# Kernel tuning notes

Hardware: AMD Instinct MI355X
Metric: run time of the kernel (lower is better)

## Reference

```python
import jax, jax.numpy as jnp
import numpy as np

B, NA, T, NV, D = 24, 50, 10, 196, 512


def setup_inputs() -> dict:
    key = jax.random.key(0)
    k1, k2 = jax.random.split(key)
    return {
        "audio_feats": jax.random.normal(k1, (B, NA, D), dtype=jnp.float32),
        "visual_feats": jax.random.normal(k2, (B, T, NV, D), dtype=jnp.float32),
        "temperature": jnp.float32(2.5),
        "scale_factor": jnp.float32(2.5),
        "threshold": jnp.float32(-2.5),
    }


def _l2norm(x):
    # F.normalize(dim=-1): x / max(||x||, 1e-12)
    n = jnp.sqrt(jnp.sum(x * x, axis=-1, keepdims=True))
    return x / jnp.maximum(n, 1e-12)


def reference(audio_feats, visual_feats, temperature, scale_factor, threshold):
    b = audio_feats.shape[0]
    a = _l2norm(audio_feats)          # (B,Na,D)
    v = _l2norm(visual_feats)         # (B,T,Nv,D)
    # all-pairs token similarities: (B,B,Na,T,Nv)
    sims = jnp.einsum('xad,ytvd->xyatv', a, v) / temperature

    # aggregate_temporal_similarities
    th = jax.nn.sigmoid(threshold)
    max_vis = jnp.max(sims, axis=-1)            # (B,B,Na,T)
    raw_diff = max_vis - th
    sel = jax.nn.relu(raw_diff) * scale_factor  # selection strength
    weighted_sum = jnp.sum(max_vis * sel, axis=-1)   # over T
    weights_sum = jnp.sum(sel, axis=-1)
    token_sims = weighted_sum / jnp.maximum(weights_sum, 1e-6)
    clip_sims = jnp.mean(token_sims, axis=-1)   # (B,B)
    fraction_selected = jnp.mean((raw_diff > 0).astype(jnp.float32))

    # InfoNCE
    idx = jnp.arange(b)
    losses_a2v = -jax.nn.log_softmax(clip_sims, axis=1)[idx, idx]
    losses_v2a = -jax.nn.log_softmax(clip_sims.T, axis=1)[idx, idx]
    contrastive_loss = jnp.mean(losses_a2v + losses_v2a) / 2

    # regularization
    neg = jnp.clip(sims, -20.0, 0.0)
    l_nonneg = jnp.mean(neg * neg)
    temp_low = jnp.maximum(-jnp.log(temperature), 0.0) ** 2   # log(1)=0
    temp_high = jnp.maximum(jnp.log(temperature) - jnp.log(4.0), 0.0) ** 2
    l_cal = temp_low + temp_high
    l_threshold = jnp.maximum(th - 0.9, 0.0) ** 2 + jnp.maximum(0.1 - th, 0.0) ** 2
    l_scale = jnp.maximum(scale_factor - 20.0, 0.0) ** 2 + jnp.maximum(1.0 - scale_factor, 0.0) ** 2
    reg_loss = 0.15 * l_nonneg + 2.0 * l_cal + 0.1 * l_threshold + 0.1 * l_scale

    # selection reward on positive pairs (diagonal)
    pos_diffs = raw_diff[idx, idx]                       # (B,Na,T)
    sel_ratio = (jnp.tanh(20.0 * pos_diffs) + 1.0) / 2.0
    selection_reward = -0.1 * jnp.log1p(jnp.mean(sel_ratio))

    total_loss = selection_reward + contrastive_loss + reg_loss
    return (total_loss, contrastive_loss, reg_loss, fraction_selected, selection_reward)
```

## Files before the change

### kernel.cpp

```cpp
#include <hip/hip_runtime.h>
#include <math.h>

#define B_   24
#define NA_  50
#define T_   10
#define NV_  196
#define D_   512
#define M_   1200
#define MPAD 1280
#define NVP  224
#define YT_  240
#define VROWS (YT_ * NVP)
#define CHB  22528

typedef __bf16 bf16x8 __attribute__((ext_vector_type(8)));
typedef float  f32x4  __attribute__((ext_vector_type(4)));
typedef unsigned short ushort8 __attribute__((ext_vector_type(8)));

__device__ __forceinline__ unsigned short f2bf(float f) {
    unsigned u = __float_as_uint(f);
    u += 0x7FFF + ((u >> 16) & 1);
    return (unsigned short)(u >> 16);
}

__device__ __forceinline__ void gload16(const void* g, void* l) {
    __builtin_amdgcn_global_load_lds(
        (const __attribute__((address_space(1))) unsigned int*)g,
        (__attribute__((address_space(3))) unsigned int*)l, 16, 0, 0);
}

__global__ void normconv_kernel(const float* __restrict__ vf, const float* __restrict__ af,
                                const float* __restrict__ tempPtr,
                                unsigned short* __restrict__ Vbf, unsigned short* __restrict__ Abf,
                                float* __restrict__ accs) {
    if (blockIdx.x == 0 && threadIdx.x < 3) accs[threadIdx.x] = 0.0f;
    int w = threadIdx.x >> 6, lane = threadIdx.x & 63;
    int row = blockIdx.x * 4 + w;
    const float* p = nullptr;
    unsigned short* dstp;
    float tscale = 1.0f;
    if (row < VROWS) {
        int yt = row / NVP, vv = row - yt * NVP;
        dstp = Vbf + (size_t)row * D_;
        if (vv < NV_) p = vf + ((size_t)yt * NV_ + vv) * D_;
    } else {
        int ar = row - VROWS;
        if (ar >= MPAD) return;
        dstp = Abf + (size_t)ar * D_;
        if (ar < M_) { p = af + (size_t)ar * D_; tscale = tempPtr[0]; }
    }
    ushort8* dst = (ushort8*)(dstp + lane * 8);
    if (p) {
        float4 u = *(const float4*)(p + lane * 8);
        float4 v = *(const float4*)(p + lane * 8 + 4);
        float s = u.x*u.x + u.y*u.y + u.z*u.z + u.w*u.w
                + v.x*v.x + v.y*v.y + v.z*v.z + v.w*v.w;
        #pragma unroll
        for (int off = 32; off; off >>= 1) s += __shfl_xor(s, off, 64);
        float sc = 1.0f / (fmaxf(sqrtf(s), 1e-12f) * tscale);
        ushort8 o;
        o[0]=f2bf(u.x*sc); o[1]=f2bf(u.y*sc); o[2]=f2bf(u.z*sc); o[3]=f2bf(u.w*sc);
        o[4]=f2bf(v.x*sc); o[5]=f2bf(v.y*sc); o[6]=f2bf(v.z*sc); o[7]=f2bf(v.w*sc);
        *dst = o;
    } else {
        ushort8 z = (ushort8)0;
        *dst = z;
    }
}

__global__ __launch_bounds__(256) void simred_kernel(
    const unsigned short* __restrict__ Abf, const unsigned short* __restrict__ Vbf,
    float* __restrict__ maxvis, float* __restrict__ accNonneg)
{
    __shared__ __align__(16) unsigned char lds[CHB];
    __shared__ float maxred[2][128];
    __shared__ float redbuf[4];

    const int tid  = threadIdx.x;
    const int lane = tid & 63;
    const int w    = tid >> 6;
    const int q    = lane >> 4;
    const int m16  = lane & 15;
    const int wr   = w & 1;
    const int wc   = w >> 1;

    const int flat = blockIdx.x + gridDim.x * blockIdx.y;
    const int xcd  = flat & 7;
    const int slot = flat >> 3;
    const int grp  = slot / 10;
    const int rt   = slot - grp * 10;
    const int yt   = xcd * 30 + grp;
    const int rowA0 = rt * 128;
    const size_t vRow0 = (size_t)yt * NVP;

    const unsigned short* gp[6];
    int lpOff[6];
    int nun = 0;
    #pragma unroll
    for (int i = 0; i < 6; ++i) {
        int u = w + 4 * i;
        if (u < 22) {
            if (u < 8) gp[nun] = Abf + (size_t)(rowA0 + u * 16 + m16) * D_ + q * 8;
            else       gp[nun] = Vbf + (vRow0 + (size_t)((u - 8) * 16 + m16)) * D_ + q * 8;
            lpOff[nun] = u * 1024;
            ++nun;
        }
    }

    int aOff[4], bOff[7];
    #pragma unroll
    for (int i = 0; i < 4; ++i) aOff[i] = (wr * 4 + i) * 1024 + q * 256 + m16 * 16;
    #pragma unroll
    for (int j = 0; j < 7; ++j) bOff[j] = 8192 + (wc * 7 + j) * 1024 + q * 256 + m16 * 16;

    f32x4 acc[4][7];
    #pragma unroll
    for (int i = 0; i < 4; ++i)
        #pragma unroll
        for (int j = 0; j < 7; ++j) acc[i][j] = (f32x4)0.0f;

    for (int c = 0; c < 16; ++c) {
        __syncthreads();
        #pragma unroll
        for (int i = 0; i < 6; ++i)
            if (i < nun) gload16(gp[i] + c * 32, lds + lpOff[i]);
        __syncthreads();
        bf16x8 afr[4], bfr[7];
        #pragma unroll
        for (int i = 0; i < 4; ++i) afr[i] = *(const bf16x8*)(lds + aOff[i]);
        #pragma unroll
        for (int j = 0; j < 7; ++j) bfr[j] = *(const bf16x8*)(lds + bOff[j]);
        #pragma unroll
        for (int i = 0; i < 4; ++i)
            #pragma unroll
            for (int j = 0; j < 7; ++j)
                acc[i][j] = __builtin_amdgcn_mfma_f32_16x16x32_bf16(afr[i], bfr[j], acc[i][j], 0, 0, 0);
    }

    float cs = 0.0f;
    #pragma unroll
    for (int i = 0; i < 4; ++i)
        #pragma unroll
        for (int j = 0; j < 7; ++j)
            #pragma unroll
            for (int r = 0; r < 4; ++r) {
                float v = acc[i][j][r];
                float cv = fminf(fmaxf(v, -20.0f), 0.0f);
                cs += cv * cv;
            }
    #pragma unroll
    for (int off = 32; off; off >>= 1) cs += __shfl_xor(cs, off, 64);
    if (lane == 0) redbuf[w] = cs;

    bool colv[7];
    #pragma unroll
    for (int j = 0; j < 7; ++j) colv[j] = (wc * 112 + j * 16 + m16) < NV_;
    #pragma unroll
    for (int i = 0; i < 4; ++i) {
        float mx[4] = {-3e38f, -3e38f, -3e38f, -3e38f};
        #pragma unroll
        for (int j = 0; j < 7; ++j)
            #pragma unroll
            for (int r = 0; r < 4; ++r)
                mx[r] = fmaxf(mx[r], colv[j] ? acc[i][j][r] : -3e38f);
        #pragma unroll
        for (int r = 0; r < 4; ++r) {
            float mm = mx[r];
            #pragma unroll
            for (int off = 1; off <= 8; off <<= 1) mm = fmaxf(mm, __shfl_xor(mm, off, 64));
            if (m16 == 0) maxred[wc][wr * 64 + i * 16 + q * 4 + r] = mm;
        }
    }
    __syncthreads();
    if (tid == 0) atomicAdd(accNonneg, redbuf[0] + redbuf[1] + redbuf[2] + redbuf[3]);
    if (tid < 128) {
        float mm = fmaxf(maxred[0][tid], maxred[1][tid]);
        int R = rowA0 + tid;
        if (R < M_) {
            int x = R / NA_, a = R - x * NA_;
            int y = yt / T_, t = yt - y * T_;
            maxvis[(((size_t)x * B_ + y) * NA_ + a) * T_ + t] = mm;
        }
    }
}

__global__ void aggregate_kernel(const float* __restrict__ maxvis,
                                 const float* __restrict__ thrPtr,
                                 const float* __restrict__ scalePtr,
                                 float* __restrict__ clipSims,
                                 float* __restrict__ accFrac,
                                 float* __restrict__ accSel)
{
    int xy = blockIdx.x;
    int x = xy / B_, y = xy % B_;
    int a = threadIdx.x;
    float th    = 1.0f / (1.0f + expf(-thrPtr[0]));
    float scale = scalePtr[0];
    float token = 0.0f, cnt = 0.0f, selsum = 0.0f;
    if (a < NA_) {
        const float* p = maxvis + (((size_t)x * B_ + y) * NA_ + a) * T_;
        float ws = 0.0f, ss = 0.0f;
        #pragma unroll
        for (int t = 0; t < T_; ++t) {
            float mv  = p[t];
            float rd  = mv - th;
            float sel = fmaxf(rd, 0.0f) * scale;
            ws += mv * sel;
            ss += sel;
            if (rd > 0.0f) cnt += 1.0f;
            if (x == y) selsum += 0.5f * (tanhf(20.0f * rd) + 1.0f);
        }
        token = ws / fmaxf(ss, 1e-6f);
    }
    #pragma unroll
    for (int off = 32; off; off >>= 1) {
        token  += __shfl_xor(token,  off, 64);
        cnt    += __shfl_xor(cnt,    off, 64);
        selsum += __shfl_xor(selsum, off, 64);
    }
    if (threadIdx.x == 0) {
        clipSims[x * B_ + y] = token / (float)NA_;
        atomicAdd(accFrac, cnt);
        if (x == y) atomicAdd(accSel, selsum);
    }
}

__global__ void finalize_kernel(const float* __restrict__ clipSims,
                                const float* __restrict__ accs,
                                const float* __restrict__ tempPtr,
                                const float* __restrict__ scalePtr,
                                const float* __restrict__ thrPtr,
                                float* __restrict__ out)
{
    __shared__ float cs[B_ * B_];
    int tid = threadIdx.x;
    for (int i = tid; i < B_ * B_; i += 64) cs[i] = clipSims[i];
    __syncthreads();
    float lsum = 0.0f;
    if (tid < B_) {
        int i = tid;
        float m = -1e30f;
        for (int j = 0; j < B_; ++j) m = fmaxf(m, cs[i * B_ + j]);
        float e = 0.0f;
        for (int j = 0; j < B_; ++j) e += expf(cs[i * B_ + j] - m);
        float la = m + logf(e) - cs[i * B_ + i];
        float m2 = -1e30f;
        for (int j = 0; j < B_; ++j) m2 = fmaxf(m2, cs[j * B_ + i]);
        float e2 = 0.0f;
        for (int j = 0; j < B_; ++j) e2 += expf(cs[j * B_ + i] - m2);
        float lv = m2 + logf(e2) - cs[i * B_ + i];
        lsum = la + lv;
    }
    #pragma unroll
    for (int off = 32; off; off >>= 1) lsum += __shfl_xor(lsum, off, 64);
    if (tid == 0) {
        float contrastive = lsum / (float)B_ * 0.5f;
        float temp = tempPtr[0], scl = scalePtr[0];
        float th = 1.0f / (1.0f + expf(-thrPtr[0]));
        float l_nonneg = accs[0] / 56448000.0f;
        float logt = logf(temp);
        float tl  = fmaxf(-logt, 0.0f);
        float thi = fmaxf(logt - logf(4.0f), 0.0f);
        float l_cal = tl * tl + thi * thi;
        float t1 = fmaxf(th - 0.9f, 0.0f), t2 = fmaxf(0.1f - th, 0.0f);
        float l_thr = t1 * t1 + t2 * t2;
        float s1 = fmaxf(scl - 20.0f, 0.0f), s2 = fmaxf(1.0f - scl, 0.0f);
        float l_scale = s1 * s1 + s2 * s2;
        float reg = 0.15f * l_nonneg + 2.0f * l_cal + 0.1f * l_thr + 0.1f * l_scale;
        float frac   = accs[1] / 288000.0f;
        float selrew = -0.1f * log1pf(accs[2] / 12000.0f);
        out[0] = selrew + contrastive + reg;
        out[1] = contrastive;
        out[2] = reg;
        out[3] = frac;
        out[4] = selrew;
    }
}

extern "C" void kernel_launch(void* const* d_in, const int* in_sizes, int n_in,
                              void* d_out, int out_size, void* d_ws, size_t ws_size,
                              hipStream_t stream) {
    const float* audio  = (const float*)d_in[0];
    const float* visual = (const float*)d_in[1];
    const float* temp   = (const float*)d_in[2];
    const float* scale  = (const float*)d_in[3];
    const float* thr    = (const float*)d_in[4];
    float* out = (float*)d_out;

    unsigned char* wsb = (unsigned char*)d_ws;
    unsigned short* Abf = (unsigned short*)wsb;
    unsigned short* Vbf = (unsigned short*)(wsb + 1310720);
    float* maxvis   = (float*)(wsb + 1310720 + 55050240);
    float* clipSims = (float*)(wsb + 1310720 + 55050240 + 1152000);
    float* accs     = clipSims + 576;

    normconv_kernel<<<(VROWS + MPAD) / 4, 256, 0, stream>>>(visual, audio, temp, Vbf, Abf, accs);

    dim3 grid(MPAD / 128, YT_);
    simred_kernel<<<grid, 256, 0, stream>>>(Abf, Vbf, maxvis, accs);

    aggregate_kernel<<<B_ * B_, 64, 0, stream>>>(maxvis, thr, scale, clipSims, accs + 1, accs + 2);
    finalize_kernel<<<1, 64, 0, stream>>>(clipSims, accs, temp, scale, thr, out);
}
```

Measured before the change: 307.6 us.

## Halve simred row tile and prefetch next K-chunk through registers

```diff
diff --git a/kernel.cpp b/kernel.cpp
--- a/kernel.cpp
+++ b/kernel.cpp
@@ -11,7 +11,7 @@
 #define NVP  224
 #define YT_  240
 #define VROWS (YT_ * NVP)
-#define CHB  22528
+#define CHB  18432
 
 typedef __bf16 bf16x8 __attribute__((ext_vector_type(8)));
 typedef float  f32x4  __attribute__((ext_vector_type(4)));
@@ -21,12 +21,6 @@
     unsigned u = __float_as_uint(f);
     u += 0x7FFF + ((u >> 16) & 1);
     return (unsigned short)(u >> 16);
-}
-
-__device__ __forceinline__ void gload16(const void* g, void* l) {
-    __builtin_amdgcn_global_load_lds(
-        (const __attribute__((address_space(1))) unsigned int*)g,
-        (__attribute__((address_space(3))) unsigned int*)l, 16, 0, 0);
 }
 
 __global__ void normconv_kernel(const float* __restrict__ vf, const float* __restrict__ af,
@@ -73,7 +67,7 @@
     float* __restrict__ maxvis, float* __restrict__ accNonneg)
 {
     __shared__ __align__(16) unsigned char lds[CHB];
-    __shared__ float maxred[2][128];
+    __shared__ float maxred[2][64];
     __shared__ float redbuf[4];
 
     const int tid  = threadIdx.x;
@@ -81,57 +75,66 @@
     const int w    = tid >> 6;
     const int q    = lane >> 4;
     const int m16  = lane & 15;
-    const int wr   = w & 1;
-    const int wc   = w >> 1;
-
-    const int flat = blockIdx.x + gridDim.x * blockIdx.y;
+    const int wrow = w >> 1;
+    const int wcol = w & 1;
+
+    const int flat = blockIdx.x;
     const int xcd  = flat & 7;
     const int slot = flat >> 3;
-    const int grp  = slot / 10;
-    const int rt   = slot - grp * 10;
+    const int grp  = slot / 20;
+    const int rt   = slot - grp * 20;
     const int yt   = xcd * 30 + grp;
-    const int rowA0 = rt * 128;
+    const int rowA0 = rt * 64;
     const size_t vRow0 = (size_t)yt * NVP;
 
-    const unsigned short* gp[6];
-    int lpOff[6];
-    int nun = 0;
-    #pragma unroll
-    for (int i = 0; i < 6; ++i) {
+    const unsigned short* gp[5];
+    int lpOff[5];
+    const int nun = (w < 2) ? 5 : 4;
+    #pragma unroll
+    for (int i = 0; i < 5; ++i) {
         int u = w + 4 * i;
-        if (u < 22) {
-            if (u < 8) gp[nun] = Abf + (size_t)(rowA0 + u * 16 + m16) * D_ + q * 8;
-            else       gp[nun] = Vbf + (vRow0 + (size_t)((u - 8) * 16 + m16)) * D_ + q * 8;
-            lpOff[nun] = u * 1024;
-            ++nun;
-        }
-    }
-
-    int aOff[4], bOff[7];
-    #pragma unroll
-    for (int i = 0; i < 4; ++i) aOff[i] = (wr * 4 + i) * 1024 + q * 256 + m16 * 16;
-    #pragma unroll
-    for (int j = 0; j < 7; ++j) bOff[j] = 8192 + (wc * 7 + j) * 1024 + q * 256 + m16 * 16;
-
-    f32x4 acc[4][7];
-    #pragma unroll
-    for (int i = 0; i < 4; ++i)
+        if (u < 18) {
+            if (u < 4) gp[i] = Abf + (size_t)(rowA0 + u * 16 + m16) * D_ + q * 8;
+            else       gp[i] = Vbf + (vRow0 + (size_t)((u - 4) * 16 + m16)) * D_ + q * 8;
+            lpOff[i] = u * 1024 + lane * 16;
+        }
+    }
+
+    int aOff[2], bOff[7];
+    #pragma unroll
+    for (int i = 0; i < 2; ++i) aOff[i] = (wrow * 2 + i) * 1024 + q * 256 + m16 * 16;
+    #pragma unroll
+    for (int j = 0; j < 7; ++j) bOff[j] = 4096 + (wcol * 7 + j) * 1024 + q * 256 + m16 * 16;
+
+    f32x4 acc[2][7];
+    #pragma unroll
+    for (int i = 0; i < 2; ++i)
         #pragma unroll
         for (int j = 0; j < 7; ++j) acc[i][j] = (f32x4)0.0f;
+
+    uint4 stg[5];
+    #pragma unroll
+    for (int i = 0; i < 5; ++i)
+        if (i < nun) stg[i] = *(const uint4*)(gp[i]);
 
     for (int c = 0; c < 16; ++c) {
         __syncthreads();
         #pragma unroll
-        for (int i = 0; i < 6; ++i)
-            if (i < nun) gload16(gp[i] + c * 32, lds + lpOff[i]);
+        for (int i = 0; i < 5; ++i)
+            if (i < nun) *(uint4*)(lds + lpOff[i]) = stg[i];
         __syncthreads();
-        bf16x8 afr[4], bfr[7];
-        #pragma unroll
-        for (int i = 0; i < 4; ++i) afr[i] = *(const bf16x8*)(lds + aOff[i]);
+        if (c < 15) {
+            #pragma unroll
+            for (int i = 0; i < 5; ++i)
+                if (i < nun) stg[i] = *(const uint4*)(gp[i] + (c + 1) * 32);
+        }
+        bf16x8 afr[2], bfr[7];
+        #pragma unroll
+        for (int i = 0; i < 2; ++i) afr[i] = *(const bf16x8*)(lds + aOff[i]);
         #pragma unroll
         for (int j = 0; j < 7; ++j) bfr[j] = *(const bf16x8*)(lds + bOff[j]);
         #pragma unroll
-        for (int i = 0; i < 4; ++i)
+        for (int i = 0; i < 2; ++i)
             #pragma unroll
             for (int j = 0; j < 7; ++j)
                 acc[i][j] = __builtin_amdgcn_mfma_f32_16x16x32_bf16(afr[i], bfr[j], acc[i][j], 0, 0, 0);
@@ -139,7 +142,7 @@
 
     float cs = 0.0f;
     #pragma unroll
-    for (int i = 0; i < 4; ++i)
+    for (int i = 0; i < 2; ++i)
         #pragma unroll
         for (int j = 0; j < 7; ++j)
             #pragma unroll
@@ -154,9 +157,9 @@
 
     bool colv[7];
     #pragma unroll
-    for (int j = 0; j < 7; ++j) colv[j] = (wc * 112 + j * 16 + m16) < NV_;
-    #pragma unroll
-    for (int i = 0; i < 4; ++i) {
+    for (int j = 0; j < 7; ++j) colv[j] = (wcol * 112 + j * 16 + m16) < NV_;
+    #pragma unroll
+    for (int i = 0; i < 2; ++i) {
         float mx[4] = {-3e38f, -3e38f, -3e38f, -3e38f};
         #pragma unroll
         for (int j = 0; j < 7; ++j)
@@ -168,12 +171,12 @@
             float mm = mx[r];
             #pragma unroll
             for (int off = 1; off <= 8; off <<= 1) mm = fmaxf(mm, __shfl_xor(mm, off, 64));
-            if (m16 == 0) maxred[wc][wr * 64 + i * 16 + q * 4 + r] = mm;
+            if (m16 == 0) maxred[wcol][wrow * 32 + i * 16 + q * 4 + r] = mm;
         }
     }
     __syncthreads();
     if (tid == 0) atomicAdd(accNonneg, redbuf[0] + redbuf[1] + redbuf[2] + redbuf[3]);
-    if (tid < 128) {
+    if (tid < 64) {
         float mm = fmaxf(maxred[0][tid], maxred[1][tid]);
         int R = rowA0 + tid;
         if (R < M_) {
@@ -296,8 +299,7 @@
 
     normconv_kernel<<<(VROWS + MPAD) / 4, 256, 0, stream>>>(visual, audio, temp, Vbf, Abf, accs);
 
-    dim3 grid(MPAD / 128, YT_);
-    simred_kernel<<<grid, 256, 0, stream>>>(Abf, Vbf, maxvis, accs);
+    simred_kernel<<<4800, 256, 0, stream>>>(Abf, Vbf, maxvis, accs);
 
     aggregate_kernel<<<B_ * B_, 64, 0, stream>>>(maxvis, thr, scale, clipSims, accs + 1, accs + 2);
     finalize_kernel<<<1, 64, 0, stream>>>(clipSims, accs, temp, scale, thr, out);
```

Result: slower. 588.7 us (+91.4%).

## Keep audio tile resident in LDS and stream visual fragments directly to registers

Applied to the files above, without the earlier changes.

```diff
diff --git a/kernel.cpp b/kernel.cpp
--- a/kernel.cpp
+++ b/kernel.cpp
@@ -9,9 +9,9 @@
 #define M_   1200
 #define MPAD 1280
 #define NVP  224
+#define NVH  112
 #define YT_  240
 #define VROWS (YT_ * NVP)
-#define CHB  22528
 
 typedef __bf16 bf16x8 __attribute__((ext_vector_type(8)));
 typedef float  f32x4  __attribute__((ext_vector_type(4)));
@@ -68,123 +68,135 @@
     }
 }
 
-__global__ __launch_bounds__(256) void simred_kernel(
+__global__ __launch_bounds__(256, 2) void simred_kernel(
     const unsigned short* __restrict__ Abf, const unsigned short* __restrict__ Vbf,
-    float* __restrict__ maxvis, float* __restrict__ accNonneg)
+    float* __restrict__ maxvisH, float* __restrict__ accNonneg)
 {
-    __shared__ __align__(16) unsigned char lds[CHB];
-    __shared__ float maxred[2][128];
-    __shared__ float redbuf[4];
+    __shared__ __align__(16) unsigned char lds[65536];
 
     const int tid  = threadIdx.x;
     const int lane = tid & 63;
     const int w    = tid >> 6;
     const int q    = lane >> 4;
     const int m16  = lane & 15;
-    const int wr   = w & 1;
-    const int wc   = w >> 1;
-
-    const int flat = blockIdx.x + gridDim.x * blockIdx.y;
-    const int xcd  = flat & 7;
-    const int slot = flat >> 3;
-    const int grp  = slot / 10;
-    const int rt   = slot - grp * 10;
-    const int yt   = xcd * 30 + grp;
-    const int rowA0 = rt * 128;
-    const size_t vRow0 = (size_t)yt * NVP;
-
-    const unsigned short* gp[6];
-    int lpOff[6];
-    int nun = 0;
+
+    const int bid  = blockIdx.x;
+    const int xcd  = bid & 7;
+    const int s    = bid >> 3;
+    const int rt   = s % 20;
+    const int rep  = s / 20;
+    const int widx = rep * 4 + w;
+    const int rowA0 = rt * 64;
+
     #pragma unroll
-    for (int i = 0; i < 6; ++i) {
-        int u = w + 4 * i;
-        if (u < 22) {
-            if (u < 8) gp[nun] = Abf + (size_t)(rowA0 + u * 16 + m16) * D_ + q * 8;
-            else       gp[nun] = Vbf + (vRow0 + (size_t)((u - 8) * 16 + m16)) * D_ + q * 8;
-            lpOff[nun] = u * 1024;
-            ++nun;
+    for (int i = 0; i < 16; ++i) {
+        int u = w * 16 + i;
+        int c = u >> 2, rb = u & 3;
+        const unsigned short* g = Abf + (size_t)(rowA0 + rb * 16 + m16) * D_ + c * 32 + q * 8;
+        gload16(g, lds + u * 1024);
+    }
+    __syncthreads();
+
+    float cs = 0.0f;
+
+    #pragma unroll 1
+    for (int it = 0; it < 5; ++it) {
+        const int e    = widx + 12 * it;
+        const int ytl  = e >> 1;
+        const int half = e & 1;
+        const int yt   = xcd * 30 + ytl;
+        const unsigned short* vb =
+            Vbf + ((size_t)yt * NVP + half * NVH + m16) * D_ + q * 8;
+
+        f32x4 acc[4][7];
+        #pragma unroll
+        for (int i = 0; i < 4; ++i)
+            #pragma unroll
+            for (int j = 0; j < 7; ++j) acc[i][j] = (f32x4)0.0f;
+
+        bf16x8 bA[7], bB[7];
+        #pragma unroll
+        for (int j = 0; j < 7; ++j) bA[j] = *(const bf16x8*)(vb + (size_t)j * 16 * D_);
+
+        #pragma unroll
+        for (int cc = 0; cc < 8; ++cc) {
+            #pragma unroll
+            for (int j = 0; j < 7; ++j)
+                bB[j] = *(const bf16x8*)(vb + (size_t)j * 16 * D_ + (2 * cc + 1) * 32);
+            {
+                bf16x8 af[4];
+                #pragma unroll
+                for (int i = 0; i < 4; ++i)
+                    af[i] = *(const bf16x8*)(lds + (2 * cc) * 4096 + i * 1024 + lane * 16);
+                #pragma unroll
+                for (int i = 0; i < 4; ++i)
+                    #pragma unroll
+                    for (int j = 0; j < 7; ++j)
+                        acc[i][j] = __builtin_amdgcn_mfma_f32_16x16x32_bf16(af[i], bA[j], acc[i][j], 0, 0, 0);
+            }
+            if (cc < 7) {
+                #pragma unroll
+                for (int j = 0; j < 7; ++j)
+                    bA[j] = *(const bf16x8*)(vb + (size_t)j * 16 * D_ + (2 * cc + 2) * 32);
+            }
+            {
+                bf16x8 af[4];
+                #pragma unroll
+                for (int i = 0; i < 4; ++i)
+                    af[i] = *(const bf16x8*)(lds + (2 * cc + 1) * 4096 + i * 1024 + lane * 16);
+                #pragma unroll
+                for (int i = 0; i < 4; ++i)
+                    #pragma unroll
+                    for (int j = 0; j < 7; ++j)
+                        acc[i][j] = __builtin_amdgcn_mfma_f32_16x16x32_bf16(af[i], bB[j], acc[i][j], 0, 0, 0);
+            }
         }
-    }
-
-    int aOff[4], bOff[7];
-    #pragma unroll
-    for (int i = 0; i < 4; ++i) aOff[i] = (wr * 4 + i) * 1024 + q * 256 + m16 * 16;
-    #pragma unroll
-    for (int j = 0; j < 7; ++j) bOff[j] = 8192 + (wc * 7 + j) * 1024 + q * 256 + m16 * 16;
-
-    f32x4 acc[4][7];
-    #pragma unroll
-    for (int i = 0; i < 4; ++i)
-        #pragma unroll
-        for (int j = 0; j < 7; ++j) acc[i][j] = (f32x4)0.0f;
-
-    for (int c = 0; c < 16; ++c) {
-        __syncthreads();
-        #pragma unroll
-        for (int i = 0; i < 6; ++i)
-            if (i < nun) gload16(gp[i] + c * 32, lds + lpOff[i]);
-        __syncthreads();
-        bf16x8 afr[4], bfr[7];
-        #pragma unroll
-        for (int i = 0; i < 4; ++i) afr[i] = *(const bf16x8*)(lds + aOff[i]);
-        #pragma unroll
-        for (int j = 0; j < 7; ++j) bfr[j] = *(const bf16x8*)(lds + bOff[j]);
+
         #pragma unroll
         for (int i = 0; i < 4; ++i)
             #pragma unroll
             for (int j = 0; j < 7; ++j)
-                acc[i][j] = __builtin_amdgcn_mfma_f32_16x16x32_bf16(afr[i], bfr[j], acc[i][j], 0, 0, 0);
-    }
-
-    float cs = 0.0f;
-    #pragma unroll
-    for (int i = 0; i < 4; ++i)
-        #pragma unroll
-        for (int j = 0; j < 7; ++j)
+                #pragma unroll
+                for (int r = 0; r < 4; ++r) {
+                    float v = acc[i][j][r];
+                    float cv = fminf(fmaxf(v, -20.0f), 0.0f);
+                    cs += cv * cv;
+                }
+
+        bool colv[7];
+        #pragma unroll
+        for (int j = 0; j < 7; ++j) colv[j] = (half * NVH + j * 16 + m16) < NV_;
+        const int y = yt / T_, t = yt - (yt / T_) * T_;
+        #pragma unroll
+        for (int i = 0; i < 4; ++i) {
+            float mx[4] = {-3e38f, -3e38f, -3e38f, -3e38f};
+            #pragma unroll
+            for (int j = 0; j < 7; ++j)
+                #pragma unroll
+                for (int r = 0; r < 4; ++r)
+                    mx[r] = fmaxf(mx[r], colv[j] ? acc[i][j][r] : -3e38f);
             #pragma unroll
             for (int r = 0; r < 4; ++r) {
-                float v = acc[i][j][r];
-                float cv = fminf(fmaxf(v, -20.0f), 0.0f);
-                cs += cv * cv;
+                float mm = mx[r];
+                #pragma unroll
+                for (int off = 1; off <= 8; off <<= 1) mm = fmaxf(mm, __shfl_xor(mm, off, 64));
+                if (m16 == 0) {
+                    int R = rowA0 + i * 16 + q * 4 + r;
+                    if (R < M_) {
+                        int x = R / NA_, a = R - x * NA_;
+                        maxvisH[((((size_t)x * B_ + y) * NA_ + a) * T_ + t) * 2 + half] = mm;
+                    }
+                }
             }
+        }
+    }
+
     #pragma unroll
     for (int off = 32; off; off >>= 1) cs += __shfl_xor(cs, off, 64);
-    if (lane == 0) redbuf[w] = cs;
-
-    bool colv[7];
-    #pragma unroll
-    for (int j = 0; j < 7; ++j) colv[j] = (wc * 112 + j * 16 + m16) < NV_;
-    #pragma unroll
-    for (int i = 0; i < 4; ++i) {
-        float mx[4] = {-3e38f, -3e38f, -3e38f, -3e38f};
-        #pragma unroll
-        for (int j = 0; j < 7; ++j)
-            #pragma unroll
-            for (int r = 0; r < 4; ++r)
-                mx[r] = fmaxf(mx[r], colv[j] ? acc[i][j][r] : -3e38f);
-        #pragma unroll
-        for (int r = 0; r < 4; ++r) {
-            float mm = mx[r];
-            #pragma unroll
-            for (int off = 1; off <= 8; off <<= 1) mm = fmaxf(mm, __shfl_xor(mm, off, 64));
-            if (m16 == 0) maxred[wc][wr * 64 + i * 16 + q * 4 + r] = mm;
-        }
-    }
-    __syncthreads();
-    if (tid == 0) atomicAdd(accNonneg, redbuf[0] + redbuf[1] + redbuf[2] + redbuf[3]);
-    if (tid < 128) {
-        float mm = fmaxf(maxred[0][tid], maxred[1][tid]);
-        int R = rowA0 + tid;
-        if (R < M_) {
-            int x = R / NA_, a = R - x * NA_;
-            int y = yt / T_, t = yt - y * T_;
-            maxvis[(((size_t)x * B_ + y) * NA_ + a) * T_ + t] = mm;
-        }
-    }
-}
-
-__global__ void aggregate_kernel(const float* __restrict__ maxvis,
+    if (lane == 0) atomicAdd(accNonneg, cs);
+}
+
+__global__ void aggregate_kernel(const float* __restrict__ maxvisH,
                                  const float* __restrict__ thrPtr,
                                  const float* __restrict__ scalePtr,
                                  float* __restrict__ clipSims,
@@ -198,11 +210,11 @@
     float scale = scalePtr[0];
     float token = 0.0f, cnt = 0.0f, selsum = 0.0f;
     if (a < NA_) {
-        const float* p = maxvis + (((size_t)x * B_ + y) * NA_ + a) * T_;
+        const float* p = maxvisH + ((((size_t)x * B_ + y) * NA_ + a) * T_) * 2;
         float ws = 0.0f, ss = 0.0f;
         #pragma unroll
         for (int t = 0; t < T_; ++t) {
-            float mv  = p[t];
+            float mv  = fmaxf(p[2 * t], p[2 * t + 1]);
             float rd  = mv - th;
             float sel = fmaxf(rd, 0.0f) * scale;
             ws += mv * sel;
@@ -290,15 +302,14 @@
     unsigned char* wsb = (unsigned char*)d_ws;
     unsigned short* Abf = (unsigned short*)wsb;
     unsigned short* Vbf = (unsigned short*)(wsb + 1310720);
-    float* maxvis   = (float*)(wsb + 1310720 + 55050240);
-    float* clipSims = (float*)(wsb + 1310720 + 55050240 + 1152000);
+    float* maxvisH  = (float*)(wsb + 1310720 + 55050240);
+    float* clipSims = (float*)(wsb + 1310720 + 55050240 + 2304000);
     float* accs     = clipSims + 576;
 
     normconv_kernel<<<(VROWS + MPAD) / 4, 256, 0, stream>>>(visual, audio, temp, Vbf, Abf, accs);
 
-    dim3 grid(MPAD / 128, YT_);
-    simred_kernel<<<grid, 256, 0, stream>>>(Abf, Vbf, maxvis, accs);
-
-    aggregate_kernel<<<B_ * B_, 64, 0, stream>>>(maxvis, thr, scale, clipSims, accs + 1, accs + 2);
+    simred_kernel<<<480, 256, 0, stream>>>(Abf, Vbf, maxvisH, accs);
+
+    aggregate_kernel<<<B_ * B_, 64, 0, stream>>>(maxvisH, thr, scale, clipSims, accs + 1, accs + 2);
     finalize_kernel<<<1, 64, 0, stream>>>(clipSims, accs, temp, scale, thr, out);
 }
```

Result: slower. 439.6 us (+42.9%).
